# Kernel tuning notes

Hardware: AMD Instinct MI355X
Metric: run time of the kernel (lower is better)

Reference implementation:

```python
import jax, jax.numpy as jnp
import numpy as np

N, MAX_SIZE, SPATIAL = 50000, 32, 27
CH_IN, CH_OUT = 128, 128


def setup_inputs() -> dict:
    key = jax.random.key(0)
    k1, k2, k3, k4 = jax.random.split(key, 4)
    feat_in = jax.random.normal(k1, (N, CH_IN), dtype=jnp.float32)
    select_mat = jax.random.uniform(k2, (N, MAX_SIZE, SPATIAL), dtype=jnp.float32)
    # kaiming-uniform-ish init for weight of shape [SPATIAL, CH_OUT*CH_IN]
    fan_in = CH_OUT * CH_IN
    bound = np.sqrt(6.0 / fan_in)
    weight = jax.random.uniform(k3, (SPATIAL, CH_OUT * CH_IN), dtype=jnp.float32,
                                minval=-bound, maxval=bound)
    neighbor_idx = jax.random.randint(k4, (N, MAX_SIZE), 0, N, dtype=jnp.int64)
    return {"feat_in": feat_in, "select_mat": select_mat,
            "weight": weight, "neighbor_idx": neighbor_idx}


def reference(feat_in, select_mat, weight, neighbor_idx):
    # feat_in: [N, I]; select_mat: [N, M, S]; weight: [S, O*I]; neighbor_idx: [N, M]
    ch_in = feat_in.shape[1]
    spatial = weight.shape[0]
    ch_out = weight.shape[1] // ch_in
    w = weight.reshape(spatial, ch_out, ch_in)          # [S, O, I]
    patch_feat = feat_in[neighbor_idx]                  # irregular gather -> [N, M, I]
    # Original math: out[n,o] = sum_m sum_s sel[n,m,s] * W[s,o,i] * pf[n,m,i]
    # Contract neighbor dim first to avoid the [N, M, O, I] intermediate.
    t = jnp.einsum('nms,nmi->nsi', select_mat, patch_feat)   # [N, S, I]
    feat_out = jnp.einsum('nsi,soi->no', t, w)               # [N, O]
    return feat_out[:, :, None]                              # [N, O, 1]
```

## Files before the change

kernel.cpp:

```cpp
#include <hip/hip_runtime.h>


#define N_CHI 128
#define N_SP  27
#define N_M   32
#define KDIM  (N_SP * N_CHI)
#define SEL_STRIDE (N_M * N_SP)

typedef short s16x8 __attribute__((ext_vector_type(8)));
typedef s16x8 __attribute__((may_alias)) s16x8_a;
typedef unsigned short u16x8 __attribute__((ext_vector_type(8)));
typedef u16x8 __attribute__((may_alias)) u16x8_a;
typedef unsigned int u32x2 __attribute__((ext_vector_type(2)));
typedef u32x2 __attribute__((may_alias)) u32x2_a;
typedef float f32x4 __attribute__((ext_vector_type(4)));
typedef float f32x16 __attribute__((ext_vector_type(16)));

typedef __attribute__((address_space(3))) unsigned int as3_u32;
typedef __attribute__((address_space(1))) const unsigned int as1_u32;

static __device__ __forceinline__ unsigned short f2bf(float f) {
  unsigned int u = __float_as_uint(f);
  u += 0x7FFFu + ((u >> 16) & 1u);
  return (unsigned short)(u >> 16);
}

__global__ __launch_bounds__(128) void wconv_kernel(const float* __restrict__ w,
                                                    unsigned short* __restrict__ Wt) {
  const int s = blockIdx.x;
  const int o = blockIdx.y;
  const int i = threadIdx.x;
  Wt[((size_t)o * N_SP + s) * N_CHI + i] = f2bf(w[((size_t)s * 128 + o) * N_CHI + i]);
}

__global__ __launch_bounds__(256) void phase1_kernel(
    const float* __restrict__ feat, const float* __restrict__ sel,
    const int* __restrict__ nidx, unsigned short* __restrict__ T,
    int nbase, int nend) {
  __shared__ __align__(16) unsigned short selT[4][32 * 40];
  __shared__ __align__(16) unsigned short tbuf[4][N_SP * 128];
  const int wave = threadIdx.x >> 6;
  const int lane = threadIdx.x & 63;
  const int n = nbase + (int)blockIdx.x * 4 + wave;
  if (n >= nend) return;
  unsigned short* st = selT[wave];
  unsigned short* tb = tbuf[wave];

  const float* selp = sel + (size_t)n * SEL_STRIDE;
#pragma unroll
  for (int it = 0; it < 16; ++it) {
    int e = it * 64 + lane;
    int m = e >> 5, s = e & 31;
    float v = (s < N_SP) ? selp[m * N_SP + s] : 0.0f;
    st[s * 40 + m] = f2bf(v);
  }

  const int q = lane >> 5;
  const int col = lane & 31;

  const int* ip = nidx + (size_t)n * N_M;
  int rows[16];
#pragma unroll
  for (int ks = 0; ks < 2; ++ks)
#pragma unroll
    for (int j = 0; j < 8; ++j) rows[ks * 8 + j] = ip[ks * 16 + q * 8 + j];

  const s16x8 bf0 = *(const s16x8_a*)&st[col * 40 + q * 8];
  const s16x8 bf1 = *(const s16x8_a*)&st[col * 40 + 16 + q * 8];

#pragma unroll
  for (int ti = 0; ti < 4; ++ti) {
    const int icol = ti * 32 + col;
    float fv[16];
#pragma unroll
    for (int t = 0; t < 16; ++t) fv[t] = feat[(size_t)rows[t] * N_CHI + icol];
    s16x8 af0, af1;
#pragma unroll
    for (int j = 0; j < 8; ++j) {
      af0[j] = (short)f2bf(fv[j]);
      af1[j] = (short)f2bf(fv[8 + j]);
    }
    f32x16 acc = {0.f, 0.f, 0.f, 0.f, 0.f, 0.f, 0.f, 0.f,
                  0.f, 0.f, 0.f, 0.f, 0.f, 0.f, 0.f, 0.f};
    acc = __builtin_amdgcn_mfma_f32_32x32x16_bf16(af0, bf0, acc, 0, 0, 0);
    acc = __builtin_amdgcn_mfma_f32_32x32x16_bf16(af1, bf1, acc, 0, 0, 0);
    if (col < N_SP) {
#pragma unroll
      for (int g = 0; g < 4; ++g) {
        const int sub = ti * 8 + g * 2 + q;
        const int phys = col * 128 + (((sub ^ ((col & 7) << 2))) << 2);
        u32x2 pk;
        pk[0] = (unsigned int)f2bf(acc[4 * g + 0]) | ((unsigned int)f2bf(acc[4 * g + 1]) << 16);
        pk[1] = (unsigned int)f2bf(acc[4 * g + 2]) | ((unsigned int)f2bf(acc[4 * g + 3]) << 16);
        *(u32x2_a*)&tb[phys] = pk;
      }
    }
  }

  unsigned short* Tn = T + (size_t)(n - nbase) * KDIM;
#pragma unroll
  for (int it = 0; it < 7; ++it) {
    const int P = it * 64 + lane;
    if (P < 432) {
      const int c = P >> 4;
      const int sub = (P << 1) & 31;
      const int phys = c * 128 + (((sub ^ ((c & 7) << 2))) << 2);
      *(u16x8_a*)&Tn[(size_t)P * 8] = *(const u16x8_a*)&tb[phys];
    }
  }
}

__global__ __launch_bounds__(256) void phase2_kernel(
    const unsigned short* __restrict__ T, const unsigned short* __restrict__ Wt,
    float* __restrict__ out, int nbase, int N) {
  __shared__ __align__(16) unsigned short Alds[2][128 * 64];
  __shared__ __align__(16) unsigned short Blds[2][128 * 64];
  const int tid = threadIdx.x;
  const int lane = tid & 63;
  const int wbase = tid & ~63;
  const int wave = tid >> 6;
  const int wm = wave & 1, wn = wave >> 1;
  const int quad = lane >> 4, l16 = lane & 15;
  const size_t rowbase = (size_t)blockIdx.x * 128;

  f32x4 acc[4][4];
#pragma unroll
  for (int a = 0; a < 4; ++a)
#pragma unroll
    for (int b = 0; b < 4; ++b) acc[a][b] = (f32x4){0.f, 0.f, 0.f, 0.f};

  const unsigned short* aga[4];
  const unsigned short* bga[4];
#pragma unroll
  for (int it = 0; it < 4; ++it) {
    const int slot = it * 256 + tid;
    const int r = slot >> 3, bp = slot & 7;
    aga[it] = T + (rowbase + r) * KDIM + ((bp ^ (r & 7)) << 3);
    bga[it] = Wt + (size_t)r * KDIM + ((bp ^ (r & 7)) << 3);
  }

  auto stage = [&](int buf, int k0) {
#pragma unroll
    for (int it = 0; it < 4; ++it) {
      __builtin_amdgcn_global_load_lds(
          (as1_u32*)(const void*)(aga[it] + k0),
          (as3_u32*)(void*)&Alds[buf][(it * 256 + wbase) * 8], 16, 0, 0);
      __builtin_amdgcn_global_load_lds(
          (as1_u32*)(const void*)(bga[it] + k0),
          (as3_u32*)(void*)&Blds[buf][(it * 256 + wbase) * 8], 16, 0, 0);
    }
  };

  const int NKT = KDIM / 64;
  stage(0, 0);
  __syncthreads();

  for (int kt = 0; kt < NKT; ++kt) {
    const int cur = kt & 1;
    if (kt + 1 < NKT) stage(cur ^ 1, (kt + 1) * 64);
#pragma unroll
    for (int ks = 0; ks < 2; ++ks) {
      const int bg = ks * 4 + quad;
      s16x8 af[4], bfr[4];
#pragma unroll
      for (int mt = 0; mt < 4; ++mt) {
        const int m = wm * 64 + mt * 16 + l16;
        af[mt] = *(const s16x8_a*)&Alds[cur][m * 64 + ((bg ^ (m & 7)) << 3)];
      }
#pragma unroll
      for (int nt = 0; nt < 4; ++nt) {
        const int o = wn * 64 + nt * 16 + l16;
        bfr[nt] = *(const s16x8_a*)&Blds[cur][o * 64 + ((bg ^ (o & 7)) << 3)];
      }
#pragma unroll
      for (int mt = 0; mt < 4; ++mt)
#pragma unroll
        for (int nt = 0; nt < 4; ++nt)
          acc[mt][nt] = __builtin_amdgcn_mfma_f32_16x16x32_bf16(af[mt], bfr[nt],
                                                                acc[mt][nt], 0, 0, 0);
    }
    __syncthreads();
  }

#pragma unroll
  for (int mt = 0; mt < 4; ++mt) {
    const int growb = nbase + (int)rowbase + wm * 64 + mt * 16 + quad * 4;
#pragma unroll
    for (int r = 0; r < 4; ++r) {
      const int grow = growb + r;
      if (grow < N) {
#pragma unroll
        for (int nt = 0; nt < 4; ++nt) {
          const int o = wn * 64 + nt * 16 + l16;
          out[(size_t)grow * 128 + o] = acc[mt][nt][r];
        }
      }
    }
  }
}

extern "C" void kernel_launch(void* const* d_in, const int* in_sizes, int n_in,
                              void* d_out, int out_size, void* d_ws, size_t ws_size,
                              hipStream_t stream) {
  const float* feat = (const float*)d_in[0];
  const float* sel  = (const float*)d_in[1];
  const float* wgt  = (const float*)d_in[2];
  const int*   nidx = (const int*)d_in[3];
  float* out = (float*)d_out;
  const int N = in_sizes[0] / N_CHI;

  unsigned short* Wt = (unsigned short*)d_ws;
  const size_t WT_ELEMS = (size_t)128 * KDIM;
  unsigned short* T = Wt + WT_ELEMS;

  wconv_kernel<<<dim3(N_SP, 128), 128, 0, stream>>>(wgt, Wt);

  const size_t bytes_for_T = (ws_size > WT_ELEMS * 2) ? (ws_size - WT_ELEMS * 2) : 0;
  long cap_rows = (long)(bytes_for_T / ((size_t)KDIM * 2));
  long NC = (cap_rows / 128) * 128;
  const long Nfull = (((long)N + 127) / 128) * 128;
  if (NC > Nfull) NC = Nfull;
  if (NC <= 0) return;

  for (long nb = 0; nb < N; nb += NC) {
    long rows = (long)N - nb;
    if (rows > NC) rows = NC;
    const long rows128 = ((rows + 127) / 128) * 128;
    phase1_kernel<<<dim3((unsigned)((rows + 3) / 4)), 256, 0, stream>>>(
        feat, sel, nidx, T, (int)nb, (int)(nb + rows));
    phase2_kernel<<<dim3((unsigned)(rows128 / 128)), 256, 0, stream>>>(
        T, Wt, out, (int)nb, N);
  }
}
```

Before: 543.7 us.

## Pre-convert features to bf16, shrink phase1 LDS, deepen phase2 prefetch pipeline

Adds a kernel that converts feat_in to bf16 once, so the phase1 neighbor gather reads half the bytes and skips per-gather conversion. Phase1 now loads select_mat straight into MFMA B fragments without an LDS transpose, and halves its T staging buffer by writing in two 64-channel halves, with launch bounds raised to target more occupancy. Phase2 now keeps two tiles in flight using explicit vmcnt waits and raw barriers instead of a load-then-sync pattern. The cost is an extra kernel launch, an extra bf16 feature copy in workspace, and fragile hand-written waitcnt logic.

```diff
diff --git a/kernel.cpp b/kernel.cpp
--- a/kernel.cpp
+++ b/kernel.cpp
@@ -14,6 +14,7 @@
 typedef unsigned int u32x2 __attribute__((ext_vector_type(2)));
 typedef u32x2 __attribute__((may_alias)) u32x2_a;
 typedef float f32x4 __attribute__((ext_vector_type(4)));
+typedef f32x4 __attribute__((may_alias)) f32x4_a;
 typedef float f32x16 __attribute__((ext_vector_type(16)));
 
 typedef __attribute__((address_space(3))) unsigned int as3_u32;
@@ -33,79 +34,88 @@
   Wt[((size_t)o * N_SP + s) * N_CHI + i] = f2bf(w[((size_t)s * 128 + o) * N_CHI + i]);
 }
 
-__global__ __launch_bounds__(256) void phase1_kernel(
-    const float* __restrict__ feat, const float* __restrict__ sel,
+__global__ __launch_bounds__(256) void featbf_kernel(const float* __restrict__ feat,
+                                                     unsigned short* __restrict__ fb,
+                                                     int total4) {
+  const int i = blockIdx.x * 256 + threadIdx.x;
+  if (i >= total4) return;
+  f32x4 v = *(const f32x4_a*)&feat[(size_t)i * 4];
+  u32x2 o;
+  o[0] = (unsigned int)f2bf(v[0]) | ((unsigned int)f2bf(v[1]) << 16);
+  o[1] = (unsigned int)f2bf(v[2]) | ((unsigned int)f2bf(v[3]) << 16);
+  *(u32x2_a*)&fb[(size_t)i * 4] = o;
+}
+
+__global__ __launch_bounds__(256, 6) void phase1_kernel(
+    const unsigned short* __restrict__ featbf, const float* __restrict__ sel,
     const int* __restrict__ nidx, unsigned short* __restrict__ T,
     int nbase, int nend) {
-  __shared__ __align__(16) unsigned short selT[4][32 * 40];
-  __shared__ __align__(16) unsigned short tbuf[4][N_SP * 128];
+  __shared__ __align__(16) unsigned short tbuf[4][N_SP * 64];
   const int wave = threadIdx.x >> 6;
   const int lane = threadIdx.x & 63;
   const int n = nbase + (int)blockIdx.x * 4 + wave;
   if (n >= nend) return;
-  unsigned short* st = selT[wave];
   unsigned short* tb = tbuf[wave];
-
-  const float* selp = sel + (size_t)n * SEL_STRIDE;
-#pragma unroll
-  for (int it = 0; it < 16; ++it) {
-    int e = it * 64 + lane;
-    int m = e >> 5, s = e & 31;
-    float v = (s < N_SP) ? selp[m * N_SP + s] : 0.0f;
-    st[s * 40 + m] = f2bf(v);
-  }
-
   const int q = lane >> 5;
   const int col = lane & 31;
+  const bool sv = (col < N_SP);
+
+  const float* selp = sel + (size_t)n * SEL_STRIDE;
+  s16x8 bf0, bf1;
+#pragma unroll
+  for (int j = 0; j < 8; ++j) {
+    const int m0 = q * 8 + j;
+    float v0 = sv ? selp[m0 * N_SP + col] : 0.0f;
+    float v1 = sv ? selp[(16 + m0) * N_SP + col] : 0.0f;
+    bf0[j] = (short)f2bf(v0);
+    bf1[j] = (short)f2bf(v1);
+  }
 
   const int* ip = nidx + (size_t)n * N_M;
-  int rows[16];
+  int offe[16];
 #pragma unroll
   for (int ks = 0; ks < 2; ++ks)
 #pragma unroll
-    for (int j = 0; j < 8; ++j) rows[ks * 8 + j] = ip[ks * 16 + q * 8 + j];
-
-  const s16x8 bf0 = *(const s16x8_a*)&st[col * 40 + q * 8];
-  const s16x8 bf1 = *(const s16x8_a*)&st[col * 40 + 16 + q * 8];
-
-#pragma unroll
-  for (int ti = 0; ti < 4; ++ti) {
-    const int icol = ti * 32 + col;
-    float fv[16];
-#pragma unroll
-    for (int t = 0; t < 16; ++t) fv[t] = feat[(size_t)rows[t] * N_CHI + icol];
-    s16x8 af0, af1;
-#pragma unroll
-    for (int j = 0; j < 8; ++j) {
-      af0[j] = (short)f2bf(fv[j]);
-      af1[j] = (short)f2bf(fv[8 + j]);
-    }
-    f32x16 acc = {0.f, 0.f, 0.f, 0.f, 0.f, 0.f, 0.f, 0.f,
-                  0.f, 0.f, 0.f, 0.f, 0.f, 0.f, 0.f, 0.f};
-    acc = __builtin_amdgcn_mfma_f32_32x32x16_bf16(af0, bf0, acc, 0, 0, 0);
-    acc = __builtin_amdgcn_mfma_f32_32x32x16_bf16(af1, bf1, acc, 0, 0, 0);
-    if (col < N_SP) {
-#pragma unroll
-      for (int g = 0; g < 4; ++g) {
-        const int sub = ti * 8 + g * 2 + q;
-        const int phys = col * 128 + (((sub ^ ((col & 7) << 2))) << 2);
-        u32x2 pk;
-        pk[0] = (unsigned int)f2bf(acc[4 * g + 0]) | ((unsigned int)f2bf(acc[4 * g + 1]) << 16);
-        pk[1] = (unsigned int)f2bf(acc[4 * g + 2]) | ((unsigned int)f2bf(acc[4 * g + 3]) << 16);
-        *(u32x2_a*)&tb[phys] = pk;
-      }
-    }
-  }
-
-  unsigned short* Tn = T + (size_t)(n - nbase) * KDIM;
-#pragma unroll
-  for (int it = 0; it < 7; ++it) {
-    const int P = it * 64 + lane;
-    if (P < 432) {
-      const int c = P >> 4;
-      const int sub = (P << 1) & 31;
-      const int phys = c * 128 + (((sub ^ ((c & 7) << 2))) << 2);
-      *(u16x8_a*)&Tn[(size_t)P * 8] = *(const u16x8_a*)&tb[phys];
+    for (int j = 0; j < 8; ++j)
+      offe[ks * 8 + j] = ip[ks * 16 + q * 8 + j] * N_CHI;
+
+#pragma unroll
+  for (int h = 0; h < 2; ++h) {
+#pragma unroll
+    for (int t2 = 0; t2 < 2; ++t2) {
+      const int icol = (h * 2 + t2) * 32 + col;
+      s16x8 af0, af1;
+#pragma unroll
+      for (int j = 0; j < 8; ++j) {
+        af0[j] = (short)featbf[offe[j] + icol];
+        af1[j] = (short)featbf[offe[8 + j] + icol];
+      }
+      f32x16 acc = {0.f, 0.f, 0.f, 0.f, 0.f, 0.f, 0.f, 0.f,
+                    0.f, 0.f, 0.f, 0.f, 0.f, 0.f, 0.f, 0.f};
+      acc = __builtin_amdgcn_mfma_f32_32x32x16_bf16(af0, bf0, acc, 0, 0, 0);
+      acc = __builtin_amdgcn_mfma_f32_32x32x16_bf16(af1, bf1, acc, 0, 0, 0);
+      if (sv) {
+#pragma unroll
+        for (int g = 0; g < 4; ++g) {
+          const int sub = t2 * 8 + g * 2 + q;
+          const int phys = col * 64 + (((sub ^ ((col & 7) << 1))) << 2);
+          u32x2 pk;
+          pk[0] = (unsigned int)f2bf(acc[4 * g + 0]) | ((unsigned int)f2bf(acc[4 * g + 1]) << 16);
+          pk[1] = (unsigned int)f2bf(acc[4 * g + 2]) | ((unsigned int)f2bf(acc[4 * g + 3]) << 16);
+          *(u32x2_a*)&tb[phys] = pk;
+        }
+      }
+    }
+    unsigned short* Tn = T + (size_t)(n - nbase) * KDIM + h * 64;
+#pragma unroll
+    for (int it = 0; it < 4; ++it) {
+      const int P = it * 64 + lane;
+      if (P < 216) {
+        const int c = P >> 3;
+        const int p = P & 7;
+        const int phys = c * 64 + ((((p << 1) ^ ((c & 7) << 1))) << 2);
+        *(u16x8_a*)&Tn[(size_t)c * 128 + p * 8] = *(const u16x8_a*)&tb[phys];
+      }
     }
   }
 }
@@ -151,13 +161,7 @@
     }
   };
 
-  const int NKT = KDIM / 64;
-  stage(0, 0);
-  __syncthreads();
-
-  for (int kt = 0; kt < NKT; ++kt) {
-    const int cur = kt & 1;
-    if (kt + 1 < NKT) stage(cur ^ 1, (kt + 1) * 64);
+  auto compute = [&](int cur) {
 #pragma unroll
     for (int ks = 0; ks < 2; ++ks) {
       const int bg = ks * 4 + quad;
@@ -179,7 +183,24 @@
           acc[mt][nt] = __builtin_amdgcn_mfma_f32_16x16x32_bf16(af[mt], bfr[nt],
                                                                 acc[mt][nt], 0, 0, 0);
     }
-    __syncthreads();
+  };
+
+  const int NKT = KDIM / 64;
+  stage(0, 0);
+  stage(1, 64);
+
+  for (int kt = 0; kt < NKT; ++kt) {
+    const int cur = kt & 1;
+    if (kt < NKT - 1) asm volatile("s_waitcnt vmcnt(8)" ::: "memory");
+    else              asm volatile("s_waitcnt vmcnt(0)" ::: "memory");
+    __builtin_amdgcn_s_barrier();
+    asm volatile("" ::: "memory");
+    compute(cur);
+    if (kt + 2 < NKT) {
+      asm volatile("s_waitcnt lgkmcnt(0)" ::: "memory");
+      __builtin_amdgcn_s_barrier();
+      stage(cur, (kt + 2) * 64);
+    }
   }
 
 #pragma unroll
@@ -211,11 +232,17 @@
 
   unsigned short* Wt = (unsigned short*)d_ws;
   const size_t WT_ELEMS = (size_t)128 * KDIM;
-  unsigned short* T = Wt + WT_ELEMS;
+  unsigned short* FB = Wt + WT_ELEMS;
+  const size_t FB_ELEMS = (size_t)N * N_CHI;
+  unsigned short* T = FB + FB_ELEMS;
 
   wconv_kernel<<<dim3(N_SP, 128), 128, 0, stream>>>(wgt, Wt);
-
-  const size_t bytes_for_T = (ws_size > WT_ELEMS * 2) ? (ws_size - WT_ELEMS * 2) : 0;
+  const int total4 = (int)(FB_ELEMS / 4);
+  featbf_kernel<<<dim3((unsigned)((total4 + 255) / 256)), 256, 0, stream>>>(
+      feat, FB, total4);
+
+  const size_t used = (WT_ELEMS + FB_ELEMS) * 2;
+  const size_t bytes_for_T = (ws_size > used) ? (ws_size - used) : 0;
   long cap_rows = (long)(bytes_for_T / ((size_t)KDIM * 2));
   long NC = (cap_rows / 128) * 128;
   const long Nfull = (((long)N + 127) / 128) * 128;
@@ -227,7 +254,7 @@
     if (rows > NC) rows = NC;
     const long rows128 = ((rows + 127) / 128) * 128;
     phase1_kernel<<<dim3((unsigned)((rows + 3) / 4)), 256, 0, stream>>>(
-        feat, sel, nidx, T, (int)nb, (int)(nb + rows));
+        FB, sel, nidx, T, (int)nb, (int)(nb + rows));
     phase2_kernel<<<dim3((unsigned)(rows128 / 128)), 256, 0, stream>>>(
         T, Wt, out, (int)nb, N);
   }
```

Result: faster. 497.4 us (-8.5%).
